# Kernel tuning notes

Hardware: AMD Instinct MI355X
Metric: run time of the kernel (lower is better)

## Reference

```python
import jax, jax.numpy as jnp
import numpy as np

B, L, D, H = 8, 1024, 1024, 16
K = D // H

def setup_inputs() -> dict:
    key = jax.random.key(0)
    k1, k2, k3 = jax.random.split(key, 3)
    scale = 1.0 / np.sqrt(D)
    return {
        "x": jax.random.normal(k1, (B, L, D), dtype=jnp.float32),
        "w_in": jax.random.normal(k2, (D, 3 * D), dtype=jnp.float32) * scale,
        "b_in": jnp.zeros((3 * D,), dtype=jnp.float32),
        "w_out": jax.random.normal(k3, (D, D), dtype=jnp.float32) * scale,
        "b_out": jnp.zeros((D,), dtype=jnp.float32),
    }

def reference(x, w_in, b_in, w_out, b_out):
    # Fused QKV projection: [B, L, 3D]
    qkv = x @ w_in + b_in
    q, k, v = jnp.split(qkv, 3, axis=-1)
    # [B, L, D] -> [B, H, L, K]
    def to_heads(t):
        return t.reshape(B, L, H, K).transpose(0, 2, 1, 3)
    q, k, v = to_heads(q), to_heads(k), to_heads(v)
    # Full [B, H, L, L] score matrix (non-flash, as in source)
    logits = jnp.einsum('bhlk,bhmk->bhlm', q, k) / jnp.sqrt(jnp.float32(K))
    # NOTE: the source computes softmax but then (bug, reproduced faithfully)
    # uses the raw logits in the value contraction. causal_mask defaults False.
    out = jnp.einsum('bhlm,bhmk->bhlk', logits, v)
    out = out.transpose(0, 2, 1, 3).reshape(B, L, D)
    return out @ w_out + b_out
```

## Files before the change

kernel.cpp:

```cpp
#include <hip/hip_runtime.h>
#include <hip/hip_bf16.h>


typedef __attribute__((ext_vector_type(8))) short short8;
typedef __attribute__((ext_vector_type(4))) float f32x4;

static __device__ __forceinline__ short f2bf(float f) {
  __hip_bfloat16 h = __float2bfloat16(f);
  return __builtin_bit_cast(short, h);
}
static __device__ __forceinline__ float bf2f(short s) {
  unsigned int u = ((unsigned int)(unsigned short)s) << 16;
  return __builtin_bit_cast(float, u);
}

#define GLOAD16(src, dst)                                        \
  __builtin_amdgcn_global_load_lds(                              \
      (const __attribute__((address_space(1))) void*)(src),      \
      (__attribute__((address_space(3))) void*)(dst), 16, 0, 0)
#define BAR() __builtin_amdgcn_s_barrier()
#define SCHED() __builtin_amdgcn_sched_barrier(0)
#define WAIT_VM4() asm volatile("s_waitcnt vmcnt(4)" ::: "memory")
#define WAIT_VM0() asm volatile("s_waitcnt vmcnt(0)" ::: "memory")

static __device__ __forceinline__ void transpose_body(
    const float* __restrict__ in, __hip_bfloat16* __restrict__ out,
    int R, int C, int c0, int r0, float tile[32][33]) {
  int tx = threadIdx.x & 31;
  int ty = threadIdx.x >> 5;
#pragma unroll
  for (int i = 0; i < 4; ++i)
    tile[ty + i * 8][tx] = in[(size_t)(r0 + ty + i * 8) * C + c0 + tx];
  __syncthreads();
#pragma unroll
  for (int i = 0; i < 4; ++i)
    out[(size_t)(c0 + ty + i * 8) * R + r0 + tx] =
        __float2bfloat16(tile[tx][ty + i * 8]);
}

__global__ __launch_bounds__(256) void prep_kernel(
    const float* __restrict__ x, __hip_bfloat16* __restrict__ x_bf,
    const float* __restrict__ w_in, __hip_bfloat16* __restrict__ w_inT,
    const float* __restrict__ w_out, __hip_bfloat16* __restrict__ w_outT) {
  __shared__ float tile[32][33];
  const int bx = blockIdx.x;
  if (bx < 4096) {
    size_t i = ((size_t)bx * 256 + threadIdx.x) * 8;
    float4 v0 = *(const float4*)(x + i);
    float4 v1 = *(const float4*)(x + i + 4);
    short8 o;
    o[0] = f2bf(v0.x); o[1] = f2bf(v0.y); o[2] = f2bf(v0.z); o[3] = f2bf(v0.w);
    o[4] = f2bf(v1.x); o[5] = f2bf(v1.y); o[6] = f2bf(v1.z); o[7] = f2bf(v1.w);
    *(short8*)((__hip_bfloat16*)x_bf + i) = o;
  } else if (bx < 4096 + 3072) {
    int b = bx - 4096;
    transpose_body(w_in, w_inT, 1024, 3072, (b % 96) * 32, (b / 96) * 32, tile);
  } else {
    int b = bx - 7168;
    transpose_body(w_out, w_outT, 1024, 1024, (b % 32) * 32, (b / 32) * 32, tile);
  }
}

static __device__ __forceinline__ void store_out(__hip_bfloat16* p, float v) {
  *p = __float2bfloat16(v);
}
static __device__ __forceinline__ void store_out(float* p, float v) { *p = v; }

template <typename OutT, int KD, int AS, int NBN, int NOUT, long BTB>
__global__ __launch_bounds__(256) void gemm_bt_kernel(
    const __hip_bfloat16* __restrict__ A, const __hip_bfloat16* __restrict__ Bt,
    const float* __restrict__ bias, OutT* __restrict__ C) {
  __shared__ __align__(16) __hip_bfloat16 As[3][128 * 32];
  __shared__ __align__(16) __hip_bfloat16 Bs[3][128 * 32];

  const int t = threadIdx.x;
  A += (size_t)blockIdx.y * 1024 * AS;
  Bt += (size_t)blockIdx.y * BTB;
  C += (size_t)blockIdx.y * 1024 * NOUT;

  const int xcd = blockIdx.x & 7;
  const int c = blockIdx.x >> 3;
  int bm, bn;
  if constexpr (NBN == 24) {
    const int st = c >> 4;
    const int im = (c >> 2) & 3, in_ = c & 3;
    bm = xcd * 8 + (st & 1) * 4 + im;
    bn = (st >> 1) * 4 + in_;
  } else {
    const int cpx = gridDim.x >> 3;
    const int wg = xcd * cpx + c;
    bm = wg / NBN; bn = wg % NBN;
  }
  const int m0 = bm * 128, n0 = bn * 128;

  const int w = t >> 6, lane = t & 63;
  const int wr = w >> 1, wc = w & 1;
  const int lr = lane & 15, kg = lane >> 4;

  const int g0 = w * 128 + lane;
  const int g1 = g0 + 64;
  const int r0g = g0 >> 2, j0g = (g0 & 3) ^ ((r0g >> 1) & 3);
  const int r1g = g1 >> 2, j1g = (g1 & 3) ^ ((r1g >> 1) & 3);
  const __hip_bfloat16* srcA0 = A + (size_t)(m0 + r0g) * AS + j0g * 8;
  const __hip_bfloat16* srcA1 = A + (size_t)(m0 + r1g) * AS + j1g * 8;
  const __hip_bfloat16* srcB0 = Bt + (size_t)(n0 + r0g) * KD + j0g * 8;
  const __hip_bfloat16* srcB1 = Bt + (size_t)(n0 + r1g) * KD + j1g * 8;
  const int lds0 = w * 128 * 8;
  const int lds1 = (w * 128 + 64) * 8;

  f32x4 acc[4][4] = {};
  constexpr int steps = KD / 32;

  auto stage = [&](int buf, int kt) {
    const int ko = kt * 32;
    GLOAD16(srcA0 + ko, &As[buf][lds0]);
    GLOAD16(srcA1 + ko, &As[buf][lds1]);
    GLOAD16(srcB0 + ko, &Bs[buf][lds0]);
    GLOAD16(srcB1 + ko, &Bs[buf][lds1]);
  };

  int offA[4], offB[4];
#pragma unroll
  for (int i = 0; i < 4; ++i) {
    int rowA = wr * 64 + i * 16 + lr;
    int rowB = wc * 64 + i * 16 + lr;
    offA[i] = rowA * 32 + (kg ^ ((rowA >> 1) & 3)) * 8;
    offB[i] = rowB * 32 + (kg ^ ((rowB >> 1) & 3)) * 8;
  }

  stage(0, 0);
  stage(1, 1);
  SCHED();
  WAIT_VM4();
  BAR();
  SCHED();

  int cur = 0;
#pragma unroll 1
  for (int kt = 0; kt < steps; ++kt) {
    if (kt + 2 < steps) {
      int nb = cur + 2; if (nb >= 3) nb -= 3;
      stage(nb, kt + 2);
    }
    SCHED();
    const __hip_bfloat16* Ac = As[cur];
    const __hip_bfloat16* Bc = Bs[cur];
    short8 af[4], bfv[4];
#pragma unroll
    for (int mi = 0; mi < 4; ++mi) af[mi] = *(const short8*)&Ac[offA[mi]];
#pragma unroll
    for (int ni = 0; ni < 4; ++ni) bfv[ni] = *(const short8*)&Bc[offB[ni]];
#pragma unroll
    for (int mi = 0; mi < 4; ++mi)
#pragma unroll
      for (int ni = 0; ni < 4; ++ni)
        acc[mi][ni] = __builtin_amdgcn_mfma_f32_16x16x32_bf16(
            af[mi], bfv[ni], acc[mi][ni], 0, 0, 0);
    SCHED();
    if (kt < steps - 2) WAIT_VM4(); else WAIT_VM0();
    BAR();
    SCHED();
    ++cur; if (cur == 3) cur = 0;
  }

#pragma unroll
  for (int mi = 0; mi < 4; ++mi) {
    int row0 = m0 + wr * 64 + mi * 16 + kg * 4;
#pragma unroll
    for (int ni = 0; ni < 4; ++ni) {
      int col = n0 + wc * 64 + ni * 16 + lr;
      float bv = bias[col];
#pragma unroll
      for (int r = 0; r < 4; ++r)
        store_out(&C[(size_t)(row0 + r) * NOUT + col], acc[mi][ni][r] + bv);
    }
  }
}

__global__ __launch_bounds__(256) void ktv_kernel(
    const __hip_bfloat16* __restrict__ qkv, float* __restrict__ Spart) {
  __shared__ __align__(16) float Ks[64][68];
  __shared__ __align__(16) float Vs[64][68];
  const int bh = blockIdx.x;
  const int ch = blockIdx.y;
  const int b = bh >> 4, h = bh & 15;
  const __hip_bfloat16* base = qkv + (size_t)b * 1024 * 3072;
  const int hoff = h * 64;
  const int t = threadIdx.x;
  const int i0 = (t >> 4) * 4;
  const int j0 = (t & 15) * 4;
  const int srow = t >> 2;
  const int sg0 = t & 3;

  f32x4 acc[4] = {};

  for (int c = 0; c < 2; ++c) {
    int l0 = ch * 128 + c * 64;
#pragma unroll
    for (int rep = 0; rep < 2; ++rep) {
      int g = sg0 + rep * 4;
      const __hip_bfloat16* rowp = base + (size_t)(l0 + srow) * 3072;
      short8 kv = *(const short8*)(rowp + 1024 + hoff + g * 8);
      short8 vv = *(const short8*)(rowp + 2048 + hoff + g * 8);
      f32x4 k0, k1, v0, v1;
#pragma unroll
      for (int e = 0; e < 4; ++e) {
        k0[e] = bf2f(kv[e]); k1[e] = bf2f(kv[4 + e]);
        v0[e] = bf2f(vv[e]); v1[e] = bf2f(vv[4 + e]);
      }
      *(f32x4*)&Ks[srow][g * 8] = k0;
      *(f32x4*)&Ks[srow][g * 8 + 4] = k1;
      *(f32x4*)&Vs[srow][g * 8] = v0;
      *(f32x4*)&Vs[srow][g * 8 + 4] = v1;
    }
    __syncthreads();
#pragma unroll 8
    for (int l = 0; l < 64; ++l) {
      f32x4 kq = *(const f32x4*)&Ks[l][i0];
      f32x4 vq = *(const f32x4*)&Vs[l][j0];
#pragma unroll
      for (int ii = 0; ii < 4; ++ii) acc[ii] += kq[ii] * vq;
    }
    __syncthreads();
  }

  float* Sp = Spart + ((size_t)ch * 128 + bh) * 4096;
#pragma unroll
  for (int ii = 0; ii < 4; ++ii)
#pragma unroll
    for (int jj = 0; jj < 4; ++jj)
      Sp[(i0 + ii) * 64 + j0 + jj] = acc[ii][jj];
}

__global__ __launch_bounds__(512) void ut_kernel(
    const float* __restrict__ Spart, const __hip_bfloat16* __restrict__ w_outT,
    __hip_bfloat16* __restrict__ Ut) {
  __shared__ __align__(16) __hip_bfloat16 Sl[64][72];
  const int bh = blockIdx.x;
  const int b = bh >> 4, h = bh & 15;
  const int t = threadIdx.x, w = t >> 6, lane = t & 63;
  const int lr = lane & 15, kg = lane >> 4;

#pragma unroll
  for (int rep = 0; rep < 2; ++rep) {
    int e4 = t + rep * 512;
    int row = e4 >> 4, c4 = e4 & 15;
    f32x4 s = {};
#pragma unroll
    for (int c = 0; c < 8; ++c)
      s += *(const f32x4*)&Spart[((size_t)c * 128 + bh) * 4096 + row * 64 + c4 * 4];
    s *= 0.125f;
    __hip_bfloat16* p = &Sl[row][c4 * 4];
    p[0] = __float2bfloat16(s[0]); p[1] = __float2bfloat16(s[1]);
    p[2] = __float2bfloat16(s[2]); p[3] = __float2bfloat16(s[3]);
  }
  __syncthreads();

  const __hip_bfloat16* Ap = w_outT + (size_t)(w * 128 + lr) * 1024 + h * 64 + kg * 8;
  short8 bF[4][2];
#pragma unroll
  for (int ni = 0; ni < 4; ++ni)
#pragma unroll
    for (int kk = 0; kk < 2; ++kk)
      bF[ni][kk] = *(const short8*)&Sl[ni * 16 + lr][kk * 32 + kg * 8];

  f32x4 acc[8][4] = {};
#pragma unroll
  for (int mi = 0; mi < 8; ++mi) {
#pragma unroll
    for (int kk = 0; kk < 2; ++kk) {
      short8 aF = *(const short8*)(Ap + (size_t)mi * 16 * 1024 + kk * 32);
#pragma unroll
      for (int ni = 0; ni < 4; ++ni)
        acc[mi][ni] = __builtin_amdgcn_mfma_f32_16x16x32_bf16(
            aF, bF[ni][kk], acc[mi][ni], 0, 0, 0);
    }
  }

  __hip_bfloat16* Up = Ut + (size_t)b * 1024 * 1024;
#pragma unroll
  for (int mi = 0; mi < 8; ++mi) {
    int row0 = w * 128 + mi * 16 + kg * 4;
#pragma unroll
    for (int ni = 0; ni < 4; ++ni) {
      int col = h * 64 + ni * 16 + lr;
#pragma unroll
      for (int r = 0; r < 4; ++r)
        Up[(size_t)(row0 + r) * 1024 + col] = __float2bfloat16(acc[mi][ni][r]);
    }
  }
}

extern "C" void kernel_launch(void* const* d_in, const int* in_sizes, int n_in,
                              void* d_out, int out_size, void* d_ws, size_t ws_size,
                              hipStream_t stream) {
  const float* x = (const float*)d_in[0];
  const float* w_in = (const float*)d_in[1];
  const float* b_in = (const float*)d_in[2];
  const float* w_out = (const float*)d_in[3];
  const float* b_out = (const float*)d_in[4];
  float* out = (float*)d_out;

  char* ws = (char*)d_ws;
  __hip_bfloat16* x_bf = (__hip_bfloat16*)ws;   ws += (size_t)8192 * 1024 * 2;
  __hip_bfloat16* w_inT = (__hip_bfloat16*)ws;  ws += (size_t)3072 * 1024 * 2;
  __hip_bfloat16* w_outT = (__hip_bfloat16*)ws; ws += (size_t)1024 * 1024 * 2;
  __hip_bfloat16* qkv = (__hip_bfloat16*)ws;    ws += (size_t)8192 * 3072 * 2;
  float* Spart = (float*)ws;                    ws += (size_t)8 * 128 * 64 * 64 * 4;
  __hip_bfloat16* Ut = (__hip_bfloat16*)ws;     ws += (size_t)8 * 1024 * 1024 * 2;

  prep_kernel<<<8192, 256, 0, stream>>>(x, x_bf, w_in, w_inT, w_out, w_outT);

  gemm_bt_kernel<__hip_bfloat16, 1024, 1024, 24, 3072, 0>
      <<<dim3(1536, 1), 256, 0, stream>>>(x_bf, w_inT, b_in, qkv);

  ktv_kernel<<<dim3(128, 8), 256, 0, stream>>>(qkv, Spart);

  ut_kernel<<<128, 512, 0, stream>>>(Spart, w_outT, Ut);

  gemm_bt_kernel<float, 1024, 3072, 8, 1024, 1024 * 1024>
      <<<dim3(64, 8), 256, 0, stream>>>(qkv, Ut, b_out, out);
}
```

Measured before the change: 139.1 us.

## Fuse fp32-to-bf16 conversion of x into QKV GEMM A-tile loading

The QKV GEMM now reads x directly in fp32 through registers, converts it to bf16 and writes it into swizzled LDS, so the separate x conversion pass and its bf16 workspace are removed from prep_kernel. This avoids writing and re-reading a 16MB intermediate, but the A operand now comes through register loads plus LDS stores instead of direct global-to-LDS loads, which adds VGPR pressure and changes the wait pattern. Separately, ut_kernel is split across two blocks of 256 threads per head instead of one 512-thread block, which doubles its grid.

After: 139.5 us. About the same (+0.3%).

```diff
diff --git a/kernel.cpp b/kernel.cpp
--- a/kernel.cpp
+++ b/kernel.cpp
@@ -21,7 +21,9 @@
 #define BAR() __builtin_amdgcn_s_barrier()
 #define SCHED() __builtin_amdgcn_sched_barrier(0)
 #define WAIT_VM4() asm volatile("s_waitcnt vmcnt(4)" ::: "memory")
+#define WAIT_VM2() asm volatile("s_waitcnt vmcnt(2)" ::: "memory")
 #define WAIT_VM0() asm volatile("s_waitcnt vmcnt(0)" ::: "memory")
+#define WAIT_LGKM0() asm volatile("s_waitcnt lgkmcnt(0)" ::: "memory")
 
 static __device__ __forceinline__ void transpose_body(
     const float* __restrict__ in, __hip_bfloat16* __restrict__ out,
@@ -39,24 +41,14 @@
 }
 
 __global__ __launch_bounds__(256) void prep_kernel(
-    const float* __restrict__ x, __hip_bfloat16* __restrict__ x_bf,
     const float* __restrict__ w_in, __hip_bfloat16* __restrict__ w_inT,
     const float* __restrict__ w_out, __hip_bfloat16* __restrict__ w_outT) {
   __shared__ float tile[32][33];
   const int bx = blockIdx.x;
-  if (bx < 4096) {
-    size_t i = ((size_t)bx * 256 + threadIdx.x) * 8;
-    float4 v0 = *(const float4*)(x + i);
-    float4 v1 = *(const float4*)(x + i + 4);
-    short8 o;
-    o[0] = f2bf(v0.x); o[1] = f2bf(v0.y); o[2] = f2bf(v0.z); o[3] = f2bf(v0.w);
-    o[4] = f2bf(v1.x); o[5] = f2bf(v1.y); o[6] = f2bf(v1.z); o[7] = f2bf(v1.w);
-    *(short8*)((__hip_bfloat16*)x_bf + i) = o;
-  } else if (bx < 4096 + 3072) {
-    int b = bx - 4096;
-    transpose_body(w_in, w_inT, 1024, 3072, (b % 96) * 32, (b / 96) * 32, tile);
+  if (bx < 3072) {
+    transpose_body(w_in, w_inT, 1024, 3072, (bx % 96) * 32, (bx / 96) * 32, tile);
   } else {
-    int b = bx - 7168;
+    int b = bx - 3072;
     transpose_body(w_out, w_outT, 1024, 1024, (b % 32) * 32, (b / 32) * 32, tile);
   }
 }
@@ -66,10 +58,11 @@
 }
 static __device__ __forceinline__ void store_out(float* p, float v) { *p = v; }
 
-template <typename OutT, int KD, int AS, int NBN, int NOUT, long BTB>
+template <typename OutT, typename AT, int KD, int AS, int NBN, int NOUT, long BTB>
 __global__ __launch_bounds__(256) void gemm_bt_kernel(
-    const __hip_bfloat16* __restrict__ A, const __hip_bfloat16* __restrict__ Bt,
+    const AT* __restrict__ A, const __hip_bfloat16* __restrict__ Bt,
     const float* __restrict__ bias, OutT* __restrict__ C) {
+  constexpr bool A_F32 = (sizeof(AT) == 4);
   __shared__ __align__(16) __hip_bfloat16 As[3][128 * 32];
   __shared__ __align__(16) __hip_bfloat16 Bs[3][128 * 32];
 
@@ -101,8 +94,8 @@
   const int g1 = g0 + 64;
   const int r0g = g0 >> 2, j0g = (g0 & 3) ^ ((r0g >> 1) & 3);
   const int r1g = g1 >> 2, j1g = (g1 & 3) ^ ((r1g >> 1) & 3);
-  const __hip_bfloat16* srcA0 = A + (size_t)(m0 + r0g) * AS + j0g * 8;
-  const __hip_bfloat16* srcA1 = A + (size_t)(m0 + r1g) * AS + j1g * 8;
+  const AT* srcA0 = A + (size_t)(m0 + r0g) * AS + j0g * 8;
+  const AT* srcA1 = A + (size_t)(m0 + r1g) * AS + j1g * 8;
   const __hip_bfloat16* srcB0 = Bt + (size_t)(n0 + r0g) * KD + j0g * 8;
   const __hip_bfloat16* srcB1 = Bt + (size_t)(n0 + r1g) * KD + j1g * 8;
   const int lds0 = w * 128 * 8;
@@ -111,12 +104,39 @@
   f32x4 acc[4][4] = {};
   constexpr int steps = KD / 32;
 
-  auto stage = [&](int buf, int kt) {
+  auto stageB = [&](int buf, int kt) {
     const int ko = kt * 32;
-    GLOAD16(srcA0 + ko, &As[buf][lds0]);
-    GLOAD16(srcA1 + ko, &As[buf][lds1]);
     GLOAD16(srcB0 + ko, &Bs[buf][lds0]);
     GLOAD16(srcB1 + ko, &Bs[buf][lds1]);
+  };
+  float4 a0lo, a0hi, a1lo, a1hi;
+  auto loadA = [&](int kt) {
+    if constexpr (A_F32) {
+      const float* p0 = srcA0 + kt * 32;
+      const float* p1 = srcA1 + kt * 32;
+      a0lo = *(const float4*)p0; a0hi = *(const float4*)(p0 + 4);
+      a1lo = *(const float4*)p1; a1hi = *(const float4*)(p1 + 4);
+    }
+  };
+  auto writeA = [&](int buf) {
+    if constexpr (A_F32) {
+      short8 o0, o1;
+      o0[0] = f2bf(a0lo.x); o0[1] = f2bf(a0lo.y); o0[2] = f2bf(a0lo.z);
+      o0[3] = f2bf(a0lo.w); o0[4] = f2bf(a0hi.x); o0[5] = f2bf(a0hi.y);
+      o0[6] = f2bf(a0hi.z); o0[7] = f2bf(a0hi.w);
+      o1[0] = f2bf(a1lo.x); o1[1] = f2bf(a1lo.y); o1[2] = f2bf(a1lo.z);
+      o1[3] = f2bf(a1lo.w); o1[4] = f2bf(a1hi.x); o1[5] = f2bf(a1hi.y);
+      o1[6] = f2bf(a1hi.z); o1[7] = f2bf(a1hi.w);
+      *(short8*)&As[buf][g0 * 8] = o0;
+      *(short8*)&As[buf][g1 * 8] = o1;
+    }
+  };
+  auto stageA_lds = [&](int buf, int kt) {
+    if constexpr (!A_F32) {
+      const int ko = kt * 32;
+      GLOAD16(srcA0 + ko, &As[buf][lds0]);
+      GLOAD16(srcA1 + ko, &As[buf][lds1]);
+    }
   };
 
   int offA[4], offB[4];
@@ -128,19 +148,40 @@
     offB[i] = rowB * 32 + (kg ^ ((rowB >> 1) & 3)) * 8;
   }
 
-  stage(0, 0);
-  stage(1, 1);
-  SCHED();
-  WAIT_VM4();
-  BAR();
-  SCHED();
+  if constexpr (A_F32) {
+    loadA(0);
+    stageB(0, 0);
+    float4 b0lo = a0lo, b0hi = a0hi, b1lo = a1lo, b1hi = a1hi;
+    loadA(1);
+    stageB(1, 1);
+    SCHED();
+    WAIT_VM2();
+    SCHED();
+    writeA(1);
+    a0lo = b0lo; a0hi = b0hi; a1lo = b1lo; a1hi = b1hi;
+    writeA(0);
+    WAIT_LGKM0();
+    SCHED();
+    BAR();
+    SCHED();
+  } else {
+    stageA_lds(0, 0); stageB(0, 0);
+    stageA_lds(1, 1); stageB(1, 1);
+    SCHED();
+    WAIT_VM4();
+    BAR();
+    SCHED();
+  }
 
   int cur = 0;
 #pragma unroll 1
   for (int kt = 0; kt < steps; ++kt) {
-    if (kt + 2 < steps) {
-      int nb = cur + 2; if (nb >= 3) nb -= 3;
-      stage(nb, kt + 2);
+    int nb = cur + 2; if (nb >= 3) nb -= 3;
+    const bool pf = (kt + 2 < steps);
+    if (pf) {
+      if constexpr (A_F32) loadA(kt + 2);
+      else stageA_lds(nb, kt + 2);
+      stageB(nb, kt + 2);
     }
     SCHED();
     const __hip_bfloat16* Ac = As[cur];
@@ -157,7 +198,21 @@
         acc[mi][ni] = __builtin_amdgcn_mfma_f32_16x16x32_bf16(
             af[mi], bfv[ni], acc[mi][ni], 0, 0, 0);
     SCHED();
-    if (kt < steps - 2) WAIT_VM4(); else WAIT_VM0();
+    if constexpr (A_F32) {
+      if (pf) {
+        WAIT_VM2();
+        SCHED();
+        writeA(nb);
+        WAIT_LGKM0();
+        SCHED();
+      } else {
+        WAIT_VM0();
+        WAIT_LGKM0();
+        SCHED();
+      }
+    } else {
+      if (pf) WAIT_VM4(); else WAIT_VM0();
+    }
     BAR();
     SCHED();
     ++cur; if (cur == 3) cur = 0;
@@ -232,7 +287,7 @@
       Sp[(i0 + ii) * 64 + j0 + jj] = acc[ii][jj];
 }
 
-__global__ __launch_bounds__(512) void ut_kernel(
+__global__ __launch_bounds__(256) void ut_kernel(
     const float* __restrict__ Spart, const __hip_bfloat16* __restrict__ w_outT,
     __hip_bfloat16* __restrict__ Ut) {
   __shared__ __align__(16) __hip_bfloat16 Sl[64][72];
@@ -240,10 +295,11 @@
   const int b = bh >> 4, h = bh & 15;
   const int t = threadIdx.x, w = t >> 6, lane = t & 63;
   const int lr = lane & 15, kg = lane >> 4;
-
-#pragma unroll
-  for (int rep = 0; rep < 2; ++rep) {
-    int e4 = t + rep * 512;
+  const int nbase = blockIdx.y * 512 + w * 128;
+
+#pragma unroll
+  for (int rep = 0; rep < 4; ++rep) {
+    int e4 = t + rep * 256;
     int row = e4 >> 4, c4 = e4 & 15;
     f32x4 s = {};
 #pragma unroll
@@ -256,7 +312,7 @@
   }
   __syncthreads();
 
-  const __hip_bfloat16* Ap = w_outT + (size_t)(w * 128 + lr) * 1024 + h * 64 + kg * 8;
+  const __hip_bfloat16* Ap = w_outT + (size_t)(nbase + lr) * 1024 + h * 64 + kg * 8;
   short8 bF[4][2];
 #pragma unroll
   for (int ni = 0; ni < 4; ++ni)
@@ -280,7 +336,7 @@
   __hip_bfloat16* Up = Ut + (size_t)b * 1024 * 1024;
 #pragma unroll
   for (int mi = 0; mi < 8; ++mi) {
-    int row0 = w * 128 + mi * 16 + kg * 4;
+    int row0 = nbase + mi * 16 + kg * 4;
 #pragma unroll
     for (int ni = 0; ni < 4; ++ni) {
       int col = h * 64 + ni * 16 + lr;
@@ -302,22 +358,21 @@
   float* out = (float*)d_out;
 
   char* ws = (char*)d_ws;
-  __hip_bfloat16* x_bf = (__hip_bfloat16*)ws;   ws += (size_t)8192 * 1024 * 2;
   __hip_bfloat16* w_inT = (__hip_bfloat16*)ws;  ws += (size_t)3072 * 1024 * 2;
   __hip_bfloat16* w_outT = (__hip_bfloat16*)ws; ws += (size_t)1024 * 1024 * 2;
   __hip_bfloat16* qkv = (__hip_bfloat16*)ws;    ws += (size_t)8192 * 3072 * 2;
   float* Spart = (float*)ws;                    ws += (size_t)8 * 128 * 64 * 64 * 4;
   __hip_bfloat16* Ut = (__hip_bfloat16*)ws;     ws += (size_t)8 * 1024 * 1024 * 2;
 
-  prep_kernel<<<8192, 256, 0, stream>>>(x, x_bf, w_in, w_inT, w_out, w_outT);
-
-  gemm_bt_kernel<__hip_bfloat16, 1024, 1024, 24, 3072, 0>
-      <<<dim3(1536, 1), 256, 0, stream>>>(x_bf, w_inT, b_in, qkv);
+  prep_kernel<<<4096, 256, 0, stream>>>(w_in, w_inT, w_out, w_outT);
+
+  gemm_bt_kernel<__hip_bfloat16, float, 1024, 1024, 24, 3072, 0>
+      <<<dim3(1536, 1), 256, 0, stream>>>(x, w_inT, b_in, qkv);
 
   ktv_kernel<<<dim3(128, 8), 256, 0, stream>>>(qkv, Spart);
 
-  ut_kernel<<<128, 512, 0, stream>>>(Spart, w_outT, Ut);
-
-  gemm_bt_kernel<float, 1024, 3072, 8, 1024, 1024 * 1024>
+  ut_kernel<<<dim3(128, 2), 256, 0, stream>>>(Spart, w_outT, Ut);
+
+  gemm_bt_kernel<float, __hip_bfloat16, 1024, 3072, 8, 1024, 1024 * 1024>
       <<<dim3(64, 8), 256, 0, stream>>>(qkv, Ut, b_out, out);
 }
```
